# Kernel tuning notes

Hardware: AMD Instinct MI355X
Metric: run time of the kernel (lower is better)

Reference implementation:

```python
import jax, jax.numpy as jnp
import numpy as np

B, L = 512, 16

def setup_inputs() -> dict:
    key = jax.random.key(0)
    k1, k2 = jax.random.split(key)
    y_true = jax.random.randint(k1, (B, L), 0, 2, dtype=jnp.int32)
    y_pred = jax.random.normal(k2, (B, L), dtype=jnp.float32)
    return {"y_true": y_true, "y_pred": y_pred}

def reference(y_true, y_pred):
    b = y_true.shape[0]
    yt = y_true.reshape(b, -1)
    yp = y_pred.reshape(b, -1)
    l = yp.shape[1]
    mp = (yt == 1).astype(yp.dtype)          # [B,L] positive-row mask per label
    mn = 1.0 - mp                             # [B,L] negative-row mask per label
    n_pos = mp.sum(axis=0)                    # [L]
    n_neg = mn.sum(axis=0)                    # [L]
    # Torch selects FULL rows for pos/neg then flattens, so for each label the
    # hinge pairs every element of a positive row with every element of a
    # negative row. S[i,j] = sum_{c,d} relu(1 - yp[i,c] + yp[j,d]) is shared
    # across labels; only the row masks differ per label.
    T = jax.nn.relu(1.0 - yp[:, :, None, None] + yp[None, None, :, :])  # [B,L,B,L]
    S = T.sum(axis=(1, 3))                    # [B,B]
    per_label = jnp.einsum('il,ij,jl->l', mp, S, mn)  # sum over pos rows i, neg rows j
    # weight * mean = (1/(np*nn)) * sum / (np*L * nn*L) = sum / (np^2 * nn^2 * L^2)
    denom = (n_pos * n_neg) ** 2 * (l * l)
    valid = (n_pos > 0) & (n_neg > 0)
    loss = jnp.sum(jnp.where(valid, per_label / jnp.where(valid, denom, 1.0), 0.0))
    return loss
```

## Files before the change

### kernel.cpp

```cpp
#include <hip/hip_runtime.h>

#define NROWS 512
#define NLAB  16
#define TILE  16

__global__ void auc_zero_ws(float* __restrict__ per_label) {
    if (threadIdx.x < NLAB) per_label[threadIdx.x] = 0.0f;
}

__global__ __launch_bounds__(256) void auc_pair_kernel(const int* __restrict__ yt,
                                                       const float* __restrict__ yp,
                                                       float* __restrict__ per_label) {
    __shared__ float ya[TILE][TILE];
    __shared__ float yb[TILE][TILE];
    __shared__ unsigned posA[TILE];
    __shared__ unsigned posB[TILE];
    __shared__ float acc[NLAB];

    const int i0 = blockIdx.x * TILE;
    const int j0 = blockIdx.y * TILE;
    const int t = threadIdx.x;

    {
        const int r = t >> 4, c = t & 15;
        ya[r][c] = yp[(i0 + r) * NLAB + c];
        yb[r][c] = yp[(j0 + r) * NLAB + c] + 1.0f;
    }
    if (t < TILE) {
        unsigned pa = 0u, pb = 0u;
        #pragma unroll
        for (int l = 0; l < NLAB; ++l) {
            pa |= (yt[(i0 + t) * NLAB + l] == 1) ? (1u << l) : 0u;
            pb |= (yt[(j0 + t) * NLAB + l] == 1) ? (1u << l) : 0u;
        }
        posA[t] = pa;
        posB[t] = pb;
        acc[t] = 0.0f;
    }
    __syncthreads();

    const int ti = t >> 4;
    const int tj = t & 15;

    float a[TILE], b[TILE];
    #pragma unroll
    for (int c = 0; c < TILE; ++c) a[c] = ya[ti][c];
    #pragma unroll
    for (int d = 0; d < TILE; ++d) b[d] = yb[tj][d];

    float S = 0.0f;
    #pragma unroll
    for (int d = 0; d < TILE; ++d) {
        #pragma unroll
        for (int c = 0; c < TILE; ++c) {
            S += fmaxf(b[d] - a[c], 0.0f);
        }
    }

    unsigned bits = posA[ti] & ~posB[tj];
    while (bits) {
        const int l = __ffs(bits) - 1;
        bits &= bits - 1;
        atomicAdd(&acc[l], S);
    }
    __syncthreads();

    if (t < NLAB) atomicAdd(&per_label[t], acc[t]);
}

__global__ __launch_bounds__(512) void auc_finalize(const int* __restrict__ yt,
                                                    const float* __restrict__ per_label,
                                                    float* __restrict__ out) {
    __shared__ int cnt[NLAB];
    const int t = threadIdx.x;
    if (t < NLAB) cnt[t] = 0;
    __syncthreads();

    #pragma unroll
    for (int l = 0; l < NLAB; ++l) {
        if (yt[t * NLAB + l] == 1) atomicAdd(&cnt[l], 1);
    }
    __syncthreads();

    if (t == 0) {
        double loss = 0.0;
        for (int l = 0; l < NLAB; ++l) {
            const int np_ = cnt[l];
            const int nn_ = NROWS - np_;
            if (np_ > 0 && nn_ > 0) {
                const double prod = (double)np_ * (double)nn_;
                const double denom = prod * prod * (double)(NLAB * NLAB);
                loss += (double)per_label[l] / denom;
            }
        }
        out[0] = (float)loss;
    }
}

extern "C" void kernel_launch(void* const* d_in, const int* in_sizes, int n_in,
                              void* d_out, int out_size, void* d_ws, size_t ws_size,
                              hipStream_t stream) {
    const int* y_true = (const int*)d_in[0];
    const float* y_pred = (const float*)d_in[1];
    float* out = (float*)d_out;
    float* per_label = (float*)d_ws;

    auc_zero_ws<<<1, 64, 0, stream>>>(per_label);

    dim3 grid(NROWS / TILE, NROWS / TILE);
    auc_pair_kernel<<<grid, 256, 0, stream>>>(y_true, y_pred, per_label);

    auc_finalize<<<1, NROWS, 0, stream>>>(y_true, per_label, out);
}
```

Measured before the change: 79.98 us.

## Replace global atomics with per-block partials and fused reduce-finalize kernel

Each pair block now writes its 16 per-label sums to a private workspace slot instead of atomically adding them into a shared global array. The finalize kernel reduces the 1024 partials and counts positives in parallel across 256 threads. This removes the zeroing kernel launch and contention on 16 global atomic addresses. In exchange the workspace grows to 64KB and the single-block reduce does more global reads serially.

After: 69.21 us. -13.5%, faster.

```diff
diff --git a/kernel.cpp b/kernel.cpp
--- a/kernel.cpp
+++ b/kernel.cpp
@@ -3,14 +3,11 @@
 #define NROWS 512
 #define NLAB  16
 #define TILE  16
-
-__global__ void auc_zero_ws(float* __restrict__ per_label) {
-    if (threadIdx.x < NLAB) per_label[threadIdx.x] = 0.0f;
-}
+#define NBLK  ((NROWS / TILE) * (NROWS / TILE))
 
 __global__ __launch_bounds__(256) void auc_pair_kernel(const int* __restrict__ yt,
                                                        const float* __restrict__ yp,
-                                                       float* __restrict__ per_label) {
+                                                       float* __restrict__ partial) {
     __shared__ float ya[TILE][TILE];
     __shared__ float yb[TILE][TILE];
     __shared__ unsigned posA[TILE];
@@ -65,27 +62,52 @@
     }
     __syncthreads();
 
-    if (t < NLAB) atomicAdd(&per_label[t], acc[t]);
+    const int blk = blockIdx.y * gridDim.x + blockIdx.x;
+    if (t < NLAB) partial[blk * NLAB + t] = acc[t];
 }
 
-__global__ __launch_bounds__(512) void auc_finalize(const int* __restrict__ yt,
-                                                    const float* __restrict__ per_label,
-                                                    float* __restrict__ out) {
-    __shared__ int cnt[NLAB];
+__global__ __launch_bounds__(256) void auc_reduce_finalize(const int* __restrict__ yt,
+                                                           const float* __restrict__ partial,
+                                                           float* __restrict__ out) {
+    __shared__ float lsum[16][NLAB];
+    __shared__ int lcnt[16][NLAB];
+    __shared__ float per_label[NLAB];
+
     const int t = threadIdx.x;
-    if (t < NLAB) cnt[t] = 0;
+    const int lab = t & 15;
+    const int grp = t >> 4;
+
+    float s = 0.0f;
+    for (int k = 0; k < NBLK / 16; ++k) {
+        s += partial[(grp + 16 * k) * NLAB + lab];
+    }
+    lsum[grp][lab] = s;
+
+    int c = 0;
+    for (int k = 0; k < NROWS / 16; ++k) {
+        c += (yt[(grp + 16 * k) * NLAB + lab] == 1) ? 1 : 0;
+    }
+    lcnt[grp][lab] = c;
     __syncthreads();
 
-    #pragma unroll
-    for (int l = 0; l < NLAB; ++l) {
-        if (yt[t * NLAB + l] == 1) atomicAdd(&cnt[l], 1);
+    if (t < NLAB) {
+        float ps = 0.0f;
+        int pc = 0;
+        #pragma unroll
+        for (int g = 0; g < 16; ++g) {
+            ps += lsum[g][t];
+            pc += lcnt[g][t];
+        }
+        per_label[t] = ps;
+        lcnt[0][t] = pc;
     }
     __syncthreads();
 
     if (t == 0) {
         double loss = 0.0;
+        #pragma unroll
         for (int l = 0; l < NLAB; ++l) {
-            const int np_ = cnt[l];
+            const int np_ = lcnt[0][l];
             const int nn_ = NROWS - np_;
             if (np_ > 0 && nn_ > 0) {
                 const double prod = (double)np_ * (double)nn_;
@@ -103,12 +125,10 @@
     const int* y_true = (const int*)d_in[0];
     const float* y_pred = (const float*)d_in[1];
     float* out = (float*)d_out;
-    float* per_label = (float*)d_ws;
-
-    auc_zero_ws<<<1, 64, 0, stream>>>(per_label);
+    float* partial = (float*)d_ws;
 
     dim3 grid(NROWS / TILE, NROWS / TILE);
-    auc_pair_kernel<<<grid, 256, 0, stream>>>(y_true, y_pred, per_label);
+    auc_pair_kernel<<<grid, 256, 0, stream>>>(y_true, y_pred, partial);
 
-    auc_finalize<<<1, NROWS, 0, stream>>>(y_true, per_label, out);
+    auc_reduce_finalize<<<1, 256, 0, stream>>>(y_true, partial, out);
 }
```
